# Kernel tuning notes

Hardware: AMD Instinct MI355X
Metric: run time of the kernel (lower is better)

## Reference

```python
import jax, jax.numpy as jnp
import numpy as np

N_NODES = 10000
N_EDGES = 160000
N_GRAPHS = 16
NUM_BASIS = 8
MIN_R = 0.25
MAX_R = 4.25
NUM_NEIGH = 10.0
SQRT3 = 3.0 ** 0.5


def setup_inputs() -> dict:
    key = jax.random.key(0)
    ks = jax.random.split(key, 24)
    f32 = jnp.float32
    g = lambda k, sh: jax.random.normal(k, sh, f32)
    inp = {}
    inp['x'] = g(ks[0], (N_NODES, 32))
    inp['node_attr'] = g(ks[1], (N_NODES, 16))
    inp['edge_src'] = jax.random.randint(ks[2], (N_EDGES,), 0, N_NODES)
    inp['edge_dst'] = jax.random.randint(ks[3], (N_EDGES,), 0, N_NODES)
    inp['edge_vec'] = g(ks[4], (N_EDGES, 3))
    inp['batch'] = jnp.sort(jax.random.randint(ks[5], (N_NODES,), 0, N_GRAPHS))
    # atom embedding Linear(32x0e -> 128x0e)
    inp['W_embed'] = g(ks[6], (32, 128))
    # conv1: in 128x0e, mid 128x0e+128x1o, out 128x0e+64x1o (gate input)
    inp['c1_lin1'] = g(ks[7], (128, 128))
    inp['c1_fc_w0'] = g(ks[8], (NUM_BASIS, 64))
    inp['c1_fc_w1'] = g(ks[9], (64, 64))
    inp['c1_fc_w2'] = g(ks[10], (64, 256))  # tp weight_numel = 128 + 128
    inp['c1_lin2_s'] = g(ks[11], (128, 128))
    inp['c1_lin2_v'] = g(ks[12], (128, 64))
    inp['c1_sc'] = g(ks[13], (128, 16, 128))  # FullyConnectedTP scalar path
    # conv2: in 64x0e+64x1o, mid 128x0e, out 128x0e
    inp['c2_lin1_s'] = g(ks[14], (64, 64))
    inp['c2_lin1_v'] = g(ks[15], (64, 64))
    inp['c2_fc_w0'] = g(ks[16], (NUM_BASIS, 64))
    inp['c2_fc_w1'] = g(ks[17], (64, 64))
    inp['c2_fc_w2'] = g(ks[18], (64, 128))  # tp weight_numel = 64 + 64
    inp['c2_lin2'] = g(ks[19], (128, 128))
    inp['c2_sc'] = g(ks[20], (64, 16, 128))
    # readout MLP 128 -> 128 -> 1
    inp['Wr1'] = g(ks[21], (128, 128))
    inp['Wr2'] = g(ks[22], (128, 1))
    return inp


def _lin(h, W):
    # e3nn Linear: normalized by 1/sqrt(fan_in)
    return h @ W * (W.shape[0] ** -0.5)


def _forward(x, node_attr, edge_src, edge_dst, edge_vec, batch,
             W_embed, c1_lin1, c1_fc_w0, c1_fc_w1, c1_fc_w2, c1_lin2_s,
             c1_lin2_v, c1_sc, c2_lin1_s, c2_lin1_v, c2_fc_w0, c2_fc_w1,
             c2_fc_w2, c2_lin2, c2_sc, Wr1, Wr2):
    silu = jax.nn.silu
    inv = NUM_NEIGH ** -0.5
    # ---- edge embeddings ----
    d = jnp.linalg.norm(edge_vec, axis=1)
    c = MAX_R - MIN_R
    xs = d - MIN_R
    safe = jnp.where(xs > 0, xs, 1.0)
    kpi = jnp.arange(1, NUM_BASIS + 1, dtype=jnp.float32) * jnp.pi
    bess = (2.0 / c) ** 0.5 * jnp.sin(kpi * safe[:, None] / c) / safe[:, None]
    mask = ((xs > 0) & (xs < c)).astype(jnp.float32)[:, None]
    edge_scalars = bess * mask * (NUM_BASIS ** 0.5)  # [E, 8]
    unit = edge_vec / jnp.where(d > 0, d, 1.0)[:, None]
    sh_v = SQRT3 * unit  # l=1 SH, component normalization (l=0 SH is 1)

    # ---- atom embedding ----
    s = _lin(x, W_embed)  # [N,128] 128x0e

    # ---- layer 1: Convolution(128x0e -> 128x0e+64x1o) + Gate ----
    h = _lin(s, c1_lin1)
    w = silu(_lin(edge_scalars, c1_fc_w0))
    w = silu(_lin(w, c1_fc_w1))
    w = _lin(w, c1_fc_w2)  # [E,256] per-edge TP weights
    w0, w1 = w[:, :128], w[:, 128:]
    hs = h[edge_src]  # gather [E,128]
    e_s = w0 * hs                                   # 0e x 0e -> 0e
    e_v = (w1 * hs)[:, :, None] * sh_v[:, None, :]  # 0e x 1o -> 1o  [E,128,3]
    n_s = jax.ops.segment_sum(e_s, edge_dst, num_segments=N_NODES) * inv
    n_v = jax.ops.segment_sum(e_v, edge_dst, num_segments=N_NODES) * inv
    out_s = _lin(n_s, c1_lin2_s)  # [N,128]: 64 scalars + 64 gates
    out_v = jnp.einsum('nui,uv->nvi', n_v, c1_lin2_v) * (128 ** -0.5)  # [N,64,3]
    sc1 = jnp.einsum('nu,nv,uvw->nw', s, node_attr, c1_sc) * ((128 * 16) ** -0.5)
    out_s = out_s + sc1
    g_s = silu(out_s[:, :64])                                  # gated scalars
    g_v = jax.nn.sigmoid(out_s[:, 64:])[:, :, None] * out_v    # gated 64x1o

    # ---- layer 2: final Convolution(64x0e+64x1o -> 128x0e) ----
    h_s = _lin(g_s, c2_lin1_s)
    h_v = jnp.einsum('nui,uv->nvi', g_v, c2_lin1_v) * (64 ** -0.5)
    w = silu(_lin(edge_scalars, c2_fc_w0))
    w = silu(_lin(w, c2_fc_w1))
    w = _lin(w, c2_fc_w2)  # [E,128]
    w0, w1 = w[:, :64], w[:, 64:]
    es = w0 * h_s[edge_src]                                           # 0e x 0e -> 0e
    ed = w1 * jnp.einsum('eui,ei->eu', h_v[edge_src], sh_v) * (3.0 ** -0.5)  # 1o x 1o -> 0e
    e_mid = jnp.concatenate([es, ed], axis=1)  # [E,128]
    n_mid = jax.ops.segment_sum(e_mid, edge_dst, num_segments=N_NODES) * inv
    out = _lin(n_mid, c2_lin2)
    sc2 = jnp.einsum('nu,nv,uvw->nw', g_s, node_attr, c2_sc) * ((64 * 16) ** -0.5)
    out = out + sc2  # [N,128]

    # ---- readout: mean pool per graph, MLP -> scalar per graph ----
    cnt = jax.ops.segment_sum(jnp.ones((N_NODES,), jnp.float32), batch,
                              num_segments=N_GRAPHS)
    pooled = jax.ops.segment_sum(out, batch, num_segments=N_GRAPHS)
    pooled = pooled / jnp.maximum(cnt, 1.0)[:, None]
    r = silu(_lin(pooled, Wr1))
    r = _lin(r, Wr2)  # [G,1]
    return r.reshape(-1)  # [G]


def reference(x, node_attr, edge_src, edge_dst, edge_vec, batch,
              W_embed, c1_lin1, c1_fc_w0, c1_fc_w1, c1_fc_w2, c1_lin2_s,
              c1_lin2_v, c1_sc, c2_lin1_s, c2_lin1_v, c2_fc_w0, c2_fc_w1,
              c2_fc_w2, c2_lin2, c2_sc, Wr1, Wr2):
    return _forward(x, node_attr, edge_src, edge_dst, edge_vec, batch,
                    W_embed, c1_lin1, c1_fc_w0, c1_fc_w1, c1_fc_w2, c1_lin2_s,
                    c1_lin2_v, c1_sc, c2_lin1_s, c2_lin1_v, c2_fc_w0, c2_fc_w1,
                    c2_fc_w2, c2_lin2, c2_sc, Wr1, Wr2)
```

## Files before the change

### kernel.cpp

```cpp
#include <hip/hip_runtime.h>
#include <hip/hip_fp16.h>

#define N_NODES 10000
#define N_EDGES 160000
#define N_GRAPHS 16

typedef __attribute__((ext_vector_type(8))) _Float16 f16x8;
typedef __attribute__((ext_vector_type(4))) float f32x4;
typedef __attribute__((ext_vector_type(4))) unsigned short u16x4;
typedef __attribute__((ext_vector_type(2))) unsigned short u16x2;
typedef unsigned int uint32;
typedef unsigned short u16;

#define OFF_ES8  0
#define OFF_SHV  (OFF_ES8 + N_EDGES*8)
#define OFF_S    (OFF_SHV + N_EDGES*3)
#define OFF_H    (OFF_S   + N_NODES*128)
#define OFF_GS   (OFF_H   + N_NODES*128)
#define OFF_HS   (OFF_GS  + N_NODES*64)
#define OFF_HV   (OFF_HS  + N_NODES*64)
#define OFF_NS   (OFF_HV  + N_NODES*192)
#define OFF_NV   (OFF_NS  + N_NODES*128)
#define OFF_NMID (OFF_NV  + N_NODES*384)
#define OFF_POOL (OFF_NMID+ N_NODES*128)
#define OFF_CNT  (OFF_POOL+ N_GRAPHS*128)
#define OFF_HIST (OFF_CNT + N_GRAPHS)
#define OFF_CURS (OFF_HIST+ N_NODES)
#define OFF_OFFS (OFF_CURS+ N_NODES)
#define OFF_FRAG (OFF_OFFS+ N_NODES + 16)
#define OFF_SLOT (OFF_FRAG+ 57344)
#define OFF_WBUF (OFF_SLOT+ N_EDGES)
#define WBUF_FLOATS ((size_t)N_EDGES*256)
#define WS_NEED_BYTES ((size_t)(OFF_WBUF + WBUF_FLOATS) * 4)

#define F_B1   0
#define F_B2   2048
#define F_B3   6144
#define F_B1b  22528
#define F_B2b  24576
#define F_B3b  28672
#define F_WE   36864
#define F_L1   40960
#define FRAG_TOT 57344

#define NF_WLS 0
#define NF_C1  16384
#define NF_W2  278528
#define NF_C2  294912
#define NF_LV  425984
#define NF_2S  434176
#define NF_2V  438272
#define NFRAG_TOT 442368

#define NM128 (N_NODES*128)

#define INV_SQRT32   0.17677669529663687f
#define INV_SQRT128  0.08838834764831845f
#define INV_SQRT8    0.3535533905932738f
#define INV_SQRT64   0.125f
#define INV_SQRT2048 0.022097086912079608f
#define INV_SQRT1024 0.03125f
#define INV_SQRT10   0.31622776601683794f
#define INV_SQRT3    0.5773502691896258f
#define SQRT3_C      1.7320508075688772f

__device__ __forceinline__ float siluf(float x){ return x / (1.f + __expf(-x)); }
__device__ __forceinline__ float sigf (float x){ return 1.f / (1.f + __expf(-x)); }
__device__ __forceinline__ u16 f2h(float x){ return __half_as_ushort(__float2half_rn(x)); }
__device__ __forceinline__ float h2f(u16 b){ return __half2float(__ushort_as_half(b)); }
__device__ __forceinline__ f16x8 cvt8(const float* __restrict__ p) {
  f32x4 v0 = *(const f32x4*)p;
  f32x4 v1 = *(const f32x4*)(p + 4);
  f16x8 r;
  r[0]=(_Float16)v0[0]; r[1]=(_Float16)v0[1]; r[2]=(_Float16)v0[2]; r[3]=(_Float16)v0[3];
  r[4]=(_Float16)v1[0]; r[5]=(_Float16)v1[1]; r[6]=(_Float16)v1[2]; r[7]=(_Float16)v1[3];
  return r;
}

__device__ __forceinline__ void geom_core(const float* __restrict__ ev,
                                          float* __restrict__ es, float* __restrict__ sv) {
  float vx = ev[0], vy = ev[1], vz = ev[2];
  float d  = sqrtf(vx*vx + vy*vy + vz*vz);
  float xs = d - 0.25f;
  bool  in = (xs > 0.f) && (xs < 4.0f);
  float safe = xs > 0.f ? xs : 1.f;
  float amp  = in ? 2.0f/safe : 0.f;
  const float PI4 = 0.7853981633974483f;
  #pragma unroll
  for (int k = 0; k < 8; ++k)
    es[k] = amp * sinf((float)(k+1) * PI4 * safe);
  float invd = d > 0.f ? 1.f/d : 1.f;
  sv[0] = SQRT3_C*vx*invd;
  sv[1] = SQRT3_C*vy*invd;
  sv[2] = SQRT3_C*vz*invd;
}

__global__ void k_geom_csr(const float* __restrict__ evec, const int* __restrict__ slot,
                           float* __restrict__ es8, float* __restrict__ shv) {
  int p = blockIdx.x*256 + threadIdx.x;
  if (p >= N_EDGES) return;
  int e = slot[p];
  float es[8], sv[3];
  geom_core(evec + (size_t)e*3, es, sv);
  #pragma unroll
  for (int k = 0; k < 8; ++k) es8[(size_t)p*8+k] = es[k];
  shv[(size_t)p*3+0] = sv[0]; shv[(size_t)p*3+1] = sv[1]; shv[(size_t)p*3+2] = sv[2];
}

__global__ void k_geom_id(const float* __restrict__ evec,
                          float* __restrict__ es8, float* __restrict__ shv) {
  int e = blockIdx.x*256 + threadIdx.x;
  if (e >= N_EDGES) return;
  float es[8], sv[3];
  geom_core(evec + (size_t)e*3, es, sv);
  #pragma unroll
  for (int k = 0; k < 8; ++k) es8[(size_t)e*8+k] = es[k];
  shv[(size_t)e*3+0] = sv[0]; shv[(size_t)e*3+1] = sv[1]; shv[(size_t)e*3+2] = sv[2];
}

__global__ void k_linear128(const float* __restrict__ A, const float* __restrict__ W,
                            float* __restrict__ O, int K, float scale, int total) {
  int t = blockIdx.x*256 + threadIdx.x;
  if (t >= total) return;
  int n = t >> 7, j = t & 127;
  const float* a = A + n*K;
  float a0=0.f,a1=0.f,a2=0.f,a3=0.f;
  for (int k = 0; k < K; k += 4) {
    a0 += a[k+0]*W[(k+0)*128+j];
    a1 += a[k+1]*W[(k+1)*128+j];
    a2 += a[k+2]*W[(k+2)*128+j];
    a3 += a[k+3]*W[(k+3)*128+j];
  }
  O[t] = (a0+a1+a2+a3)*scale;
}

__global__ void k_cnthist(const int* __restrict__ batch, const int* __restrict__ edst,
                          float* __restrict__ cnt, int* __restrict__ hist) {
  __shared__ int lc[N_GRAPHS];
  int t = threadIdx.x;
  if (t < N_GRAPHS) lc[t] = 0;
  __syncthreads();
  int i = blockIdx.x*256 + t;
  if (i < N_NODES) atomicAdd(&lc[batch[i]], 1);
  if (i < N_EDGES) atomicAdd(&hist[edst[i]], 1);
  __syncthreads();
  if (t < N_GRAPHS && lc[t] > 0) atomicAdd(&cnt[t], (float)lc[t]);
}

__global__ __launch_bounds__(1024) void k_scanp(const int* __restrict__ hist,
                                                int* __restrict__ offs) {
  __shared__ int wsum[16];
  const int t = threadIdx.x;
  const int lane = t & 63, w = t >> 6;
  const int base = t*10;
  int v[10]; int s = 0;
  #pragma unroll
  for (int i = 0; i < 10; ++i) {
    int idx = base + i;
    int x = (idx < N_NODES) ? hist[idx] : 0;
    s += x; v[i] = s;
  }
  int ws = s;
  #pragma unroll
  for (int d = 1; d < 64; d <<= 1) {
    int u = __shfl_up(ws, d);
    if (lane >= d) ws += u;
  }
  if (lane == 63) wsum[w] = ws;
  __syncthreads();
  if (w == 0) {
    int x = (lane < 16) ? wsum[lane] : 0;
    #pragma unroll
    for (int d = 1; d < 16; d <<= 1) {
      int u = __shfl_up(x, d);
      if (lane >= d) x += u;
    }
    if (lane < 16) wsum[lane] = x;
  }
  __syncthreads();
  int waveoff = (w > 0) ? wsum[w-1] : 0;
  int texcl = waveoff + ws - s;
  if (t == 0) offs[0] = 0;
  #pragma unroll
  for (int i = 0; i < 10; ++i) {
    int idx = base + i;
    if (idx < N_NODES) offs[idx+1] = texcl + v[i];
  }
}

__global__ void k_slot(const int* __restrict__ edst, const int* __restrict__ esrc,
                       const int* __restrict__ offs,
                       int* __restrict__ curs, int* __restrict__ slot,
                       int* __restrict__ esrcp) {
  int e = blockIdx.x*256 + threadIdx.x;
  if (e < N_EDGES) {
    int d = edst[e];
    int p = offs[d] + atomicAdd(&curs[d], 1);
    slot[p] = e;
    esrcp[p] = esrc[e];
  }
}

struct PD { const float* W; u16* dst; int Keff, N, KS, nElem; float scale; };
struct PD8 { PD d[8]; int nd; int tot; };

__global__ void k_prepmulti(PD8 ds) {
  int stride = gridDim.x*256;
  for (int t = blockIdx.x*256 + threadIdx.x; t < ds.tot; t += stride) {
    int rem = t, i = 0;
    while (i < ds.nd-1 && rem >= ds.d[i].nElem) { rem -= ds.d[i].nElem; ++i; }
    const PD p = ds.d[i];
    int j = rem & 7;
    int l = (rem >> 3) & 63;
    int rest = rem >> 9;
    int ks = rest % p.KS;
    int nf = rest / p.KS;
    int k   = ks*32 + (l >> 4)*8 + j;
    int col = nf*16 + (l & 15);
    float v = (k < p.Keff) ? p.W[(size_t)k*p.N + col]*p.scale : 0.f;
    p.dst[rem] = f2h(v);
  }
}

template<int NF3>
__global__ __launch_bounds__(256) void k_mlp(
    const float* __restrict__ es8,
    const u16* __restrict__ fb1, const u16* __restrict__ fb2,
    const u16* __restrict__ fb3, u16* __restrict__ wbuf) {
  __shared__ __align__(16) _Float16 route[4][2304];
  const int w = threadIdx.x >> 6, l = threadIdx.x & 63;
  const int lrow = l & 15, lhi = l >> 4;
  const int e0 = (blockIdx.x*4 + w)*32;
  _Float16* rt = route[w];
  constexpr int NQ = NF3/4;

  f16x8 a1[2];
  #pragma unroll
  for (int mt = 0; mt < 2; ++mt) {
    f16x8 z = {0,0,0,0,0,0,0,0};
    if (lhi == 0) z = cvt8(es8 + (size_t)(e0 + mt*16 + lrow)*8);
    a1[mt] = z;
  }

  f32x4 acc1[2][4];
  #pragma unroll
  for (int mt = 0; mt < 2; ++mt)
    #pragma unroll
    for (int nf = 0; nf < 4; ++nf) acc1[mt][nf] = (f32x4){0.f,0.f,0.f,0.f};
  #pragma unroll
  for (int nf = 0; nf < 4; ++nf) {
    f16x8 b = *(const f16x8*)(fb1 + nf*512 + l*8);
    #pragma unroll
    for (int mt = 0; mt < 2; ++mt)
      acc1[mt][nf] = __builtin_amdgcn_mfma_f32_16x16x32_f16(a1[mt], b, acc1[mt][nf], 0,0,0);
  }
  #pragma unroll
  for (int mt = 0; mt < 2; ++mt)
    #pragma unroll
    for (int nf = 0; nf < 4; ++nf)
      #pragma unroll
      for (int r = 0; r < 4; ++r) acc1[mt][nf][r] = siluf(acc1[mt][nf][r]);

  f16x8 a2[2][2];
  #pragma unroll
  for (int mt = 0; mt < 2; ++mt)
    #pragma unroll
    for (int nf = 0; nf < 4; ++nf)
      #pragma unroll
      for (int r = 0; r < 4; ++r)
        rt[(mt*16 + lhi*4 + r)*72 + nf*16 + lrow] = (_Float16)acc1[mt][nf][r];
  #pragma unroll
  for (int mt = 0; mt < 2; ++mt)
    #pragma unroll
    for (int ks = 0; ks < 2; ++ks)
      a2[mt][ks] = *(const f16x8*)&rt[(mt*16 + lrow)*72 + ks*32 + lhi*8];

  f32x4 acc2[2][4];
  #pragma unroll
  for (int mt = 0; mt < 2; ++mt)
    #pragma unroll
    for (int nf = 0; nf < 4; ++nf) acc2[mt][nf] = (f32x4){0.f,0.f,0.f,0.f};
  #pragma unroll
  for (int nf = 0; nf < 4; ++nf)
    #pragma unroll
    for (int ks = 0; ks < 2; ++ks) {
      f16x8 b = *(const f16x8*)(fb2 + (nf*2 + ks)*512 + l*8);
      #pragma unroll
      for (int mt = 0; mt < 2; ++mt)
        acc2[mt][nf] = __builtin_amdgcn_mfma_f32_16x16x32_f16(a2[mt][ks], b, acc2[mt][nf], 0,0,0);
    }
  #pragma unroll
  for (int mt = 0; mt < 2; ++mt)
    #pragma unroll
    for (int nf = 0; nf < 4; ++nf)
      #pragma unroll
      for (int r = 0; r < 4; ++r) acc2[mt][nf][r] = siluf(acc2[mt][nf][r]);

  f16x8 a3[2][2];
  #pragma unroll
  for (int mt = 0; mt < 2; ++mt)
    #pragma unroll
    for (int nf = 0; nf < 4; ++nf)
      #pragma unroll
      for (int r = 0; r < 4; ++r)
        rt[(mt*16 + lhi*4 + r)*72 + nf*16 + lrow] = (_Float16)acc2[mt][nf][r];
  #pragma unroll
  for (int mt = 0; mt < 2; ++mt)
    #pragma unroll
    for (int ks = 0; ks < 2; ++ks)
      a3[mt][ks] = *(const f16x8*)&rt[(mt*16 + lrow)*72 + ks*32 + lhi*8];

  #pragma unroll
  for (int cc = 0; cc < 4; ++cc) {
    f32x4 acc3[NQ][2];
    #pragma unroll
    for (int q = 0; q < NQ; ++q)
      #pragma unroll
      for (int mt = 0; mt < 2; ++mt) acc3[q][mt] = (f32x4){0.f,0.f,0.f,0.f};
    #pragma unroll
    for (int q = 0; q < NQ; ++q) {
      const int nf3 = q*4 + cc;
      #pragma unroll
      for (int ks = 0; ks < 2; ++ks) {
        f16x8 b = *(const f16x8*)(fb3 + ((size_t)nf3*2 + ks)*512 + l*8);
        #pragma unroll
        for (int mt = 0; mt < 2; ++mt)
          acc3[q][mt] = __builtin_amdgcn_mfma_f32_16x16x32_f16(a3[mt][ks], b, acc3[q][mt], 0,0,0);
      }
    }
    const int cbase = (cc*16 + lrow)*NQ;
    #pragma unroll
    for (int mt = 0; mt < 2; ++mt)
      #pragma unroll
      for (int r = 0; r < 4; ++r) {
        const size_t rowoff = (size_t)(e0 + mt*16 + lhi*4 + r)*(NF3*16) + cbase;
        if constexpr (NQ == 4) {
          u16x4 pk;
          #pragma unroll
          for (int q = 0; q < 4; ++q) pk[q] = f2h(acc3[q][mt][r]);
          *(u16x4*)(wbuf + rowoff) = pk;
        } else {
          u16x2 pk;
          #pragma unroll
          for (int q = 0; q < 2; ++q) pk[q] = f2h(acc3[q][mt][r]);
          *(u16x2*)(wbuf + rowoff) = pk;
        }
      }
  }
}

template<int KS, int NF>
__global__ __launch_bounds__(512, 4) void k_gemm(
    const float* __restrict__ A, int rstride, int M,
    const u16* __restrict__ fB, float* __restrict__ O) {
  __shared__ __align__(16) _Float16 lB[NF*KS*512];
  const int tid = threadIdx.x;
  const int w = tid >> 6, l = tid & 63;
  const int lrow = l & 15, lhi = l >> 4;
  const int n0 = blockIdx.x*128 + w*16;
  for (int i = tid; i < NF*KS*64; i += 512)
    *(f16x8*)&lB[(size_t)i*8] = *(const f16x8*)&fB[(size_t)i*8];
  f16x8 a[KS];
  {
    int row = n0 + lrow; if (row > M-1) row = M-1;
    #pragma unroll
    for (int ks = 0; ks < KS; ++ks)
      a[ks] = cvt8(A + (size_t)row*rstride + ks*32 + lhi*8);
  }
  __syncthreads();
  f32x4 acc[NF];
  #pragma unroll
  for (int nf = 0; nf < NF; ++nf) acc[nf] = (f32x4){0.f,0.f,0.f,0.f};
  #pragma unroll
  for (int nf = 0; nf < NF; ++nf)
    #pragma unroll
    for (int ks = 0; ks < KS; ++ks) {
      f16x8 b = *(const f16x8*)&lB[((size_t)(nf*KS + ks))*512 + l*8];
      acc[nf] = __builtin_amdgcn_mfma_f32_16x16x32_f16(a[ks], b, acc[nf], 0,0,0);
    }
  #pragma unroll
  for (int nf = 0; nf < NF; ++nf)
    #pragma unroll
    for (int r = 0; r < 4; ++r) {
      int row = n0 + lhi*4 + r;
      if (row < M) O[(size_t)row*(NF*16) + nf*16 + lrow] = acc[nf][r];
    }
}

template<int KSO>
__global__ __launch_bounds__(512, 4) void k_scp(
    const float* __restrict__ Ao, const float* __restrict__ na,
    const u16* __restrict__ fBc, float* __restrict__ part) {
  __shared__ __align__(16) _Float16 lB[KSO*4096];
  const int tid = threadIdx.x;
  const int w = tid >> 6, l = tid & 63;
  const int lrow = l & 15, lhi = l >> 4;
  const int n0 = blockIdx.x*128 + w*16;
  const int vp = blockIdx.y;

  f16x8 ao[KSO];
  {
    int row = n0 + lrow; if (row > N_NODES-1) row = N_NODES-1;
    #pragma unroll
    for (int ks = 0; ks < KSO; ++ks)
      ao[ks] = cvt8(Ao + (size_t)row*(KSO*32) + ks*32 + lhi*8);
  }

  f32x4 acc[8];
  #pragma unroll
  for (int nf = 0; nf < 8; ++nf) acc[nf] = (f32x4){0.f,0.f,0.f,0.f};

  #pragma unroll
  for (int c = 0; c < 2; ++c) {
    const int v = vp*2 + c;
    __syncthreads();
    for (int i = tid; i < KSO*512; i += 512) {
      int gl = i & 63;
      int rest = i >> 6;
      int ks = rest % KSO;
      int nf = rest / KSO;
      size_t src = (((size_t)(v*8 + nf)*KSO + ks)*64 + gl)*8;
      *(f16x8*)&lB[(size_t)i*8] = *(const f16x8*)&fBc[src];
    }
    __syncthreads();
    f32x4 dacc[8];
    #pragma unroll
    for (int nf = 0; nf < 8; ++nf) dacc[nf] = (f32x4){0.f,0.f,0.f,0.f};
    #pragma unroll
    for (int nf = 0; nf < 8; ++nf)
      #pragma unroll
      for (int ks = 0; ks < KSO; ++ks) {
        f16x8 b = *(const f16x8*)&lB[((size_t)(nf*KSO + ks))*512 + l*8];
        dacc[nf] = __builtin_amdgcn_mfma_f32_16x16x32_f16(ao[ks], b, dacc[nf], 0,0,0);
      }
    #pragma unroll
    for (int r = 0; r < 4; ++r) {
      int row = n0 + lhi*4 + r; if (row > N_NODES-1) row = N_NODES-1;
      float nav = na[(size_t)row*16 + v];
      #pragma unroll
      for (int nf = 0; nf < 8; ++nf) acc[nf][r] += nav * dacc[nf][r];
    }
  }

  float* pp = part + (size_t)vp*NM128;
  #pragma unroll
  for (int nf = 0; nf < 8; ++nf)
    #pragma unroll
    for (int r = 0; r < 4; ++r) {
      int row = n0 + lhi*4 + r;
      if (row < N_NODES) pp[(size_t)row*128 + nf*16 + lrow] = acc[nf][r];
    }
}

__global__ void k_redgate(const float* __restrict__ part, const float* __restrict__ ov,
                          float* __restrict__ gs_out, float* __restrict__ gv) {
  int t = blockIdx.x*256 + threadIdx.x;
  if (t >= N_NODES*64) return;
  int n = t >> 6, v = t & 63;
  float o1 = 0.f, o2 = 0.f;
  #pragma unroll
  for (int p = 0; p < 9; ++p) {
    const float* pp = part + (size_t)p*NM128 + (size_t)n*128;
    o1 += pp[v]; o2 += pp[64+v];
  }
  float g = siluf(o1), gate = sigf(o2);
  gs_out[(size_t)n*64+v] = g;
  gv[(size_t)n*192 + 0*64 + v] = gate*ov[(size_t)n*192 + 0*64 + v];
  gv[(size_t)n*192 + 1*64 + v] = gate*ov[(size_t)n*192 + 1*64 + v];
  gv[(size_t)n*192 + 2*64 + v] = gate*ov[(size_t)n*192 + 2*64 + v];
}

__global__ __launch_bounds__(128) void k_redpool(
    const float* __restrict__ part, const int* __restrict__ batch,
    float* __restrict__ pool) {
  const int j = threadIdx.x;
  const int n0 = blockIdx.x*4;
  float outv[4];
  #pragma unroll
  for (int nn = 0; nn < 4; ++nn) {
    float sv = 0.f;
    #pragma unroll
    for (int p = 0; p < 9; ++p)
      sv += part[(size_t)p*NM128 + (size_t)(n0+nn)*128 + j];
    outv[nn] = sv;
  }
  int b0 = batch[n0], b1 = batch[n0+1], b2 = batch[n0+2], b3 = batch[n0+3];
  float sum = outv[0]; int cur = b0;
  if (b1 == cur) sum += outv[1]; else { atomicAdd(&pool[cur*128+j], sum); cur = b1; sum = outv[1]; }
  if (b2 == cur) sum += outv[2]; else { atomicAdd(&pool[cur*128+j], sum); cur = b2; sum = outv[2]; }
  if (b3 == cur) sum += outv[3]; else { atomicAdd(&pool[cur*128+j], sum); cur = b3; sum = outv[3]; }
  atomicAdd(&pool[cur*128+j], sum);
}

__global__ __launch_bounds__(256) void k_gather1(
    const u16* __restrict__ wbuf, const float* __restrict__ shv,
    const int* __restrict__ esrcp, const int* __restrict__ offs,
    const float* __restrict__ h,
    float* __restrict__ n_s, float* __restrict__ n_v) {
  const int wave = threadIdx.x >> 6, lane = threadIdx.x & 63;
  const int n = blockIdx.x*4 + wave;
  if (n >= N_NODES) return;
  const int s0 = offs[n], s1 = offs[n+1];
  float ns0=0.f, ns1=0.f;
  float nv00=0.f,nv01=0.f,nv02=0.f, nv10=0.f,nv11=0.f,nv12=0.f;
  for (int s = s0; s < s1; ++s) {
    int src = esrcp[s];
    u16x4 wv = *(const u16x4*)(wbuf + (size_t)s*256 + lane*4);
    float c0 = h2f(wv[0]), c1 = h2f(wv[1]), c2 = h2f(wv[2]), c3 = h2f(wv[3]);
    float h0 = h[src*128+lane], h1 = h[src*128+64+lane];
    float sv0 = shv[(size_t)s*3+0], sv1 = shv[(size_t)s*3+1], sv2 = shv[(size_t)s*3+2];
    ns0 += c0*h0; ns1 += c1*h1;
    float t0 = c2*h0, t1 = c3*h1;
    nv00 += t0*sv0; nv01 += t0*sv1; nv02 += t0*sv2;
    nv10 += t1*sv0; nv11 += t1*sv1; nv12 += t1*sv2;
  }
  n_s[n*128+lane]    = ns0*INV_SQRT10;
  n_s[n*128+64+lane] = ns1*INV_SQRT10;
  float* nvp = n_v + (size_t)n*384;
  nvp[0*128+lane]    = nv00*INV_SQRT10;
  nvp[1*128+lane]    = nv01*INV_SQRT10;
  nvp[2*128+lane]    = nv02*INV_SQRT10;
  nvp[0*128+64+lane] = nv10*INV_SQRT10;
  nvp[1*128+64+lane] = nv11*INV_SQRT10;
  nvp[2*128+64+lane] = nv12*INV_SQRT10;
}

__global__ __launch_bounds__(256) void k_gather2(
    const u16* __restrict__ wbuf, const float* __restrict__ shv,
    const int* __restrict__ esrcp, const int* __restrict__ offs,
    const float* __restrict__ h_s, const float* __restrict__ h_v,
    float* __restrict__ n_mid) {
  const int wave = threadIdx.x >> 6, lane = threadIdx.x & 63;
  const int n = blockIdx.x*4 + wave;
  if (n >= N_NODES) return;
  const int s0 = offs[n], s1 = offs[n+1];
  float acc0 = 0.f, acc1 = 0.f;
  for (int s = s0; s < s1; ++s) {
    int src = esrcp[s];
    u16x2 wv = *(const u16x2*)(wbuf + (size_t)s*128 + lane*2);
    float w0 = h2f(wv[0]), w1 = h2f(wv[1]);
    float hs = h_s[src*64+lane];
    const float* hvp = h_v + (size_t)src*192;
    float sv0 = shv[(size_t)s*3+0], sv1 = shv[(size_t)s*3+1], sv2 = shv[(size_t)s*3+2];
    float dot = hvp[lane]*sv0 + hvp[64+lane]*sv1 + hvp[128+lane]*sv2;
    acc0 += w0*hs;
    acc1 += w1*dot;
  }
  n_mid[n*128+lane]    = acc0*INV_SQRT10;
  n_mid[n*128+64+lane] = acc1*INV_SQRT3*INV_SQRT10;
}

__global__ __launch_bounds__(512) void k_edge1_at(
    const float* __restrict__ es8, const float* __restrict__ shv,
    const int* __restrict__ esrc, const int* __restrict__ edst,
    const float* __restrict__ h,
    const float* __restrict__ W0, const float* __restrict__ W1, const float* __restrict__ W2,
    float* __restrict__ n_s, float* __restrict__ n_v) {
  __shared__ float lW0[512];
  __shared__ float lW1[4096];
  __shared__ float lW2[16384];
  __shared__ float lA[8][64];
  __shared__ float lB[8][64];
  for (int i = threadIdx.x; i < 512;   i += 512) lW0[i] = W0[i];
  for (int i = threadIdx.x; i < 4096;  i += 512) lW1[i] = W1[i];
  for (int i = threadIdx.x; i < 16384; i += 512) lW2[i] = W2[i];
  __syncthreads();
  const int wave = threadIdx.x >> 6, lane = threadIdx.x & 63;
  const int nw = gridDim.x * 8;
  const int e0 = blockIdx.x*8 + wave;
  const int iters = (N_EDGES + nw - 1) / nw;
  for (int it = 0; it < iters; ++it) {
    int e = e0 + it*nw;
    bool valid = e < N_EDGES;
    float a = 0.f, sv0=0.f, sv1=0.f, sv2=0.f;
    int src = 0, dst = 0;
    if (valid) {
      const float* ep = es8 + e*8;
      sv0 = shv[e*3+0]; sv1 = shv[e*3+1]; sv2 = shv[e*3+2];
      src = esrc[e]; dst = edst[e];
      a = ep[0]*lW0[lane]      + ep[1]*lW0[64+lane]  + ep[2]*lW0[128+lane] + ep[3]*lW0[192+lane]
        + ep[4]*lW0[256+lane]  + ep[5]*lW0[320+lane] + ep[6]*lW0[384+lane] + ep[7]*lW0[448+lane];
      a = siluf(a * INV_SQRT8);
    }
    lA[wave][lane] = a;
    __syncthreads();
    {
      float b0=0.f;
      #pragma unroll
      for (int k = 0; k < 64; ++k) b0 += lA[wave][k]*lW1[k*64+lane];
      lB[wave][lane] = siluf(b0 * INV_SQRT64);
    }
    __syncthreads();
    if (valid) {
      float c0=0.f,c1=0.f,c2=0.f,c3=0.f;
      #pragma unroll
      for (int k = 0; k < 64; ++k) {
        float bk = lB[wave][k];
        const float* r = lW2 + k*256;
        c0 += bk*r[lane]; c1 += bk*r[64+lane]; c2 += bk*r[128+lane]; c3 += bk*r[192+lane];
      }
      float hs0 = h[src*128 + lane];
      float hs1 = h[src*128 + 64 + lane];
      atomicAdd(&n_s[dst*128 + lane],      c0*INV_SQRT64*hs0*INV_SQRT10);
      atomicAdd(&n_s[dst*128 + 64 + lane], c1*INV_SQRT64*hs1*INV_SQRT10);
      float t0 = c2*INV_SQRT64*hs0*INV_SQRT10;
      float t1 = c3*INV_SQRT64*hs1*INV_SQRT10;
      float* nvp = n_v + dst*384;
      atomicAdd(nvp + lane*3+0, t0*sv0);
      atomicAdd(nvp + lane*3+1, t0*sv1);
      atomicAdd(nvp + lane*3+2, t0*sv2);
      atomicAdd(nvp + (64+lane)*3+0, t1*sv0);
      atomicAdd(nvp + (64+lane)*3+1, t1*sv1);
      atomicAdd(nvp + (64+lane)*3+2, t1*sv2);
    }
  }
}

__global__ __launch_bounds__(512) void k_edge2_at(
    const float* __restrict__ es8, const float* __restrict__ shv,
    const int* __restrict__ esrc, const int* __restrict__ edst,
    const float* __restrict__ h_s, const float* __restrict__ h_v,
    const float* __restrict__ W0, const float* __restrict__ W1, const float* __restrict__ W2,
    float* __restrict__ n_mid) {
  __shared__ float lW0[512];
  __shared__ float lW1[4096];
  __shared__ float lW2[8192];
  __shared__ float lA[8][64];
// ... 169 lines not shown
    acc[0] += l_nm[k]*w; acc[1] += l_nm[128+k]*w;
    acc[2] += l_nm[256+k]*w; acc[3] += l_nm[384+k]*w;
  }
  float acc2[4] = {0.f,0.f,0.f,0.f};
  for (int vt = 0; vt < 16; vt += 4) {
    float a0[4],a1[4],a2[4],a3[4];
    #pragma unroll
    for (int n = 0; n < 4; ++n) {
      a0[n]=l_na[n*16+vt]; a1[n]=l_na[n*16+vt+1];
      a2[n]=l_na[n*16+vt+2]; a3[n]=l_na[n*16+vt+3];
    }
    for (int u = 0; u < 64; ++u) {
      const float* cp = Csc + (u*16+vt)*128 + j;
      float c0=cp[0], c1=cp[128], c2=cp[256], c3=cp[384];
      float s0=l_gs[u], s1=l_gs[64+u], s2=l_gs[128+u], s3=l_gs[192+u];
      acc2[0] += s0*(a0[0]*c0 + a1[0]*c1 + a2[0]*c2 + a3[0]*c3);
      acc2[1] += s1*(a0[1]*c0 + a1[1]*c1 + a2[1]*c2 + a3[1]*c3);
      acc2[2] += s2*(a0[2]*c0 + a1[2]*c1 + a2[2]*c2 + a3[2]*c3);
      acc2[3] += s3*(a0[3]*c0 + a1[3]*c1 + a2[3]*c2 + a3[3]*c3);
    }
  }
  float outv[4];
  #pragma unroll
  for (int n = 0; n < 4; ++n)
    outv[n] = acc[n]*INV_SQRT128 + acc2[n]*INV_SQRT1024;
  int b0 = batch[n0], b1 = batch[n0+1], b2 = batch[n0+2], b3 = batch[n0+3];
  float sum = outv[0]; int cur = b0;
  if (b1 == cur) sum += outv[1]; else { atomicAdd(&pool[cur*128+j], sum); cur = b1; sum = outv[1]; }
  if (b2 == cur) sum += outv[2]; else { atomicAdd(&pool[cur*128+j], sum); cur = b2; sum = outv[2]; }
  if (b3 == cur) sum += outv[3]; else { atomicAdd(&pool[cur*128+j], sum); cur = b3; sum = outv[3]; }
  atomicAdd(&pool[cur*128+j], sum);
}

__global__ __launch_bounds__(128) void k_head(
    const float* __restrict__ pool, const float* __restrict__ cnt,
    const float* __restrict__ Wr1, const float* __restrict__ Wr2,
    float* __restrict__ out) {
  __shared__ float lp[128];
  __shared__ float wsum[2];
  const int j = threadIdx.x;
  const int g = blockIdx.x;
  float inv = 1.f / fmaxf(cnt[g], 1.f);
  lp[j] = pool[(size_t)g*128 + j]*inv;
  __syncthreads();
  float acc = 0.f;
  for (int k = 0; k < 128; ++k) acc += lp[k]*Wr1[k*128+j];
  float val = siluf(acc*INV_SQRT128) * Wr2[j];
  #pragma unroll
  for (int d = 32; d > 0; d >>= 1) val += __shfl_down(val, d);
  if ((j & 63) == 0) wsum[j >> 6] = val;
  __syncthreads();
  if (j == 0) out[g] = (wsum[0] + wsum[1]) * INV_SQRT128;
}

extern "C" void kernel_launch(void* const* d_in, const int* in_sizes, int n_in,
                              void* d_out, int out_size, void* d_ws, size_t ws_size,
                              hipStream_t stream) {
  const float* x         = (const float*)d_in[0];
  const float* node_attr = (const float*)d_in[1];
  const int*   esrc      = (const int*)d_in[2];
  const int*   edst      = (const int*)d_in[3];
  const float* evec      = (const float*)d_in[4];
  const int*   batch     = (const int*)d_in[5];
  const float* W_embed   = (const float*)d_in[6];
  const float* c1_lin1   = (const float*)d_in[7];
  const float* c1_fc_w0  = (const float*)d_in[8];
  const float* c1_fc_w1  = (const float*)d_in[9];
  const float* c1_fc_w2  = (const float*)d_in[10];
  const float* c1_lin2_s = (const float*)d_in[11];
  const float* c1_lin2_v = (const float*)d_in[12];
  const float* c1_sc     = (const float*)d_in[13];
  const float* c2_lin1_s = (const float*)d_in[14];
  const float* c2_lin1_v = (const float*)d_in[15];
  const float* c2_fc_w0  = (const float*)d_in[16];
  const float* c2_fc_w1  = (const float*)d_in[17];
  const float* c2_fc_w2  = (const float*)d_in[18];
  const float* c2_lin2   = (const float*)d_in[19];
  const float* c2_sc     = (const float*)d_in[20];
  const float* Wr1       = (const float*)d_in[21];
  const float* Wr2       = (const float*)d_in[22];

  float* ws    = (float*)d_ws;
  float* es8   = ws + OFF_ES8;
  float* shv   = ws + OFF_SHV;
  float* s_    = ws + OFF_S;
  float* h_    = ws + OFF_H;
  float* gs_   = ws + OFF_GS;
  float* hs_   = ws + OFF_HS;
  float* hv_   = ws + OFF_HV;
  float* ns_   = ws + OFF_NS;
  float* nv_   = ws + OFF_NV;
  float* nmid_ = ws + OFF_NMID;
  float* pool_ = ws + OFF_POOL;
  float* cnt_  = ws + OFF_CNT;
  int*   hist_ = (int*)(ws + OFF_HIST);
  int*   curs_ = (int*)(ws + OFF_CURS);
  int*   offs_ = (int*)(ws + OFF_OFFS);
  u16*   frag_ = (u16*)(ws + OFF_FRAG);
  int*   slot_ = (int*)(ws + OFF_SLOT);
  float* wbuf_ = ws + OFF_WBUF;
  u16*   wb16_ = (u16*)wbuf_;

  float* out1_  = wbuf_ + (size_t)N_EDGES*128;
  u16*   nfrag_ = (u16*)(out1_ + (size_t)NM128);
  float* part_  = out1_ + (size_t)NM128 + NFRAG_TOT/2;
  float* ov_    = part_ + (size_t)9*NM128;
  int*   esrcp_ = (int*)(ov_ + (size_t)N_NODES*192);
  float* gv_    = nv_;

  const bool big = ws_size >= WS_NEED_BYTES;

  if (big) {
    hipMemsetAsync(pool_, 0, (size_t)(OFF_OFFS - OFF_POOL)*sizeof(float), stream);
    k_cnthist<<<(N_EDGES+255)/256, 256, 0, stream>>>(batch, edst, cnt_, hist_);
    k_scanp<<<1, 1024, 0, stream>>>(hist_, offs_);
    k_slot<<<(N_EDGES+255)/256, 256, 0, stream>>>(edst, esrc, offs_, curs_, slot_, esrcp_);
    k_geom_csr<<<(N_EDGES+255)/256, 256, 0, stream>>>(evec, slot_, es8, shv);

    {
      PD8 m{};
      m.d[0] = {c1_fc_w0, frag_ + F_B1,  8,  64,  1, 2048,  INV_SQRT8};
      m.d[1] = {c1_fc_w1, frag_ + F_B2,  64, 64,  2, 4096,  INV_SQRT64};
      m.d[2] = {c1_fc_w2, frag_ + F_B3,  64, 256, 2, 16384, INV_SQRT64};
      m.d[3] = {c2_fc_w0, frag_ + F_B1b, 8,  64,  1, 2048,  INV_SQRT8};
      m.d[4] = {c2_fc_w1, frag_ + F_B2b, 64, 64,  2, 4096,  INV_SQRT64};
      m.d[5] = {c2_fc_w2, frag_ + F_B3b, 64, 128, 2, 8192,  INV_SQRT64};
      m.d[6] = {W_embed,  frag_ + F_WE,  32, 128, 1, 4096,  INV_SQRT32};
      m.d[7] = {c1_lin1,  frag_ + F_L1,  128,128, 4, 16384, INV_SQRT128};
      m.nd = 8; m.tot = FRAG_TOT;
      k_prepmulti<<<224, 256, 0, stream>>>(m);
    }

    k_gemm<1,8><<<79, 512, 0, stream>>>(x,  32,  N_NODES, frag_ + F_WE, s_);
    k_gemm<4,8><<<79, 512, 0, stream>>>(s_, 128, N_NODES, frag_ + F_L1, h_);

    k_mlp<16><<<1250, 256, 0, stream>>>(es8, frag_ + F_B1, frag_ + F_B2, frag_ + F_B3, wb16_);
    k_gather1<<<(N_NODES+3)/4, 256, 0, stream>>>(wb16_, shv, esrcp_, offs_, h_, ns_, nv_);

    {
      PD8 m{};
      m.d[0] = {c1_lin2_s, nfrag_ + NF_WLS, 128, 128,  4, 16384,  INV_SQRT128};
      m.d[1] = {c1_sc,     nfrag_ + NF_C1,  128, 2048, 4, 262144, INV_SQRT2048};
      m.d[2] = {c2_lin2,   nfrag_ + NF_W2,  128, 128,  4, 16384,  INV_SQRT128};
      m.d[3] = {c2_sc,     nfrag_ + NF_C2,  64,  2048, 2, 131072, INV_SQRT1024};
      m.d[4] = {c1_lin2_v, nfrag_ + NF_LV,  128, 64,   4, 8192,   INV_SQRT128};
      m.d[5] = {c2_lin1_s, nfrag_ + NF_2S,  64,  64,   2, 4096,   INV_SQRT64};
      m.d[6] = {c2_lin1_v, nfrag_ + NF_2V,  64,  64,   2, 4096,   INV_SQRT64};
      m.nd = 7; m.tot = NFRAG_TOT;
      k_prepmulti<<<864, 256, 0, stream>>>(m);
    }

    k_gemm<4,8><<<79, 512, 0, stream>>>(ns_, 128, N_NODES, nfrag_ + NF_WLS, part_ + (size_t)8*NM128);
    k_scp<4><<<dim3(79,8), 512, 0, stream>>>(s_, node_attr, nfrag_ + NF_C1, part_);
    k_gemm<4,4><<<235, 512, 0, stream>>>(nv_, 128, N_NODES*3, nfrag_ + NF_LV, ov_);
    k_redgate<<<(N_NODES*64+255)/256, 256, 0, stream>>>(part_, ov_, gs_, gv_);
    k_gemm<2,4><<<79, 512, 0, stream>>>(gs_, 64, N_NODES, nfrag_ + NF_2S, hs_);
    k_gemm<2,4><<<235, 512, 0, stream>>>(gv_, 64, N_NODES*3, nfrag_ + NF_2V, hv_);

    k_mlp<8><<<1250, 256, 0, stream>>>(es8, frag_ + F_B1b, frag_ + F_B2b, frag_ + F_B3b, wb16_);
    k_gather2<<<(N_NODES+3)/4, 256, 0, stream>>>(wb16_, shv, esrcp_, offs_, hs_, hv_, nmid_);

    k_gemm<4,8><<<79, 512, 0, stream>>>(nmid_, 128, N_NODES, nfrag_ + NF_W2, part_ + (size_t)8*NM128);
    k_scp<2><<<dim3(79,8), 512, 0, stream>>>(gs_, node_attr, nfrag_ + NF_C2, part_);
    k_redpool<<<N_NODES/4, 128, 0, stream>>>(part_, batch, pool_);
  } else {
    hipMemsetAsync(ns_, 0, (size_t)(OFF_HIST - OFF_NS)*sizeof(float), stream);
    k_geom_id<<<N_EDGES/256, 256, 0, stream>>>(evec, es8, shv);
    k_linear128<<<(N_NODES*128)/256, 256, 0, stream>>>(x,  W_embed, s_, 32,  INV_SQRT32,  N_NODES*128);
    k_linear128<<<(N_NODES*128)/256, 256, 0, stream>>>(s_, c1_lin1, h_, 128, INV_SQRT128, N_NODES*128);
    k_cnthist<<<(N_EDGES+255)/256, 256, 0, stream>>>(batch, edst, cnt_, hist_);
    k_edge1_at<<<256, 512, 0, stream>>>(es8, shv, esrc, edst, h_,
                                        c1_fc_w0, c1_fc_w1, c1_fc_w2, ns_, nv_);
    k_node1<<<N_NODES/4, 128, 0, stream>>>(ns_, nv_, s_, node_attr,
                                           c1_lin2_s, c1_lin2_v, c1_sc,
                                           c2_lin1_s, c2_lin1_v, gs_, hs_, hv_);
    k_edge2_at<<<512, 512, 0, stream>>>(es8, shv, esrc, edst, hs_, hv_,
                                        c2_fc_w0, c2_fc_w1, c2_fc_w2, nmid_);
    k_node2<<<N_NODES/4, 128, 0, stream>>>(nmid_, gs_, node_attr, batch,
                                           c2_lin2, c2_sc, pool_);
  }

  k_head<<<N_GRAPHS, 128, 0, stream>>>(pool_, cnt_, Wr1, Wr2, (float*)d_out);
}
```

Baseline: 275.4 us.

## Fuse slot and geometry kernels, merge weight prep, store gathered features as fp16

Merges the CSR slot assignment with edge geometry so each edge is handled in one kernel, and writes the radial basis as fp16 so the MLP kernel loads it directly. Combines the two weight-fragment preparation launches into one. GEMMs that produce node features read by the edge gathers (h, hs, hv) now write fp16, halving the bytes the random-access gathers fetch. This trades precision in the gathered features for less memory traffic and fewer launches.

Measured after the change: 261.3 us (median of 2 runs). 5.1% less time.

```diff
diff --git a/kernel.cpp b/kernel.cpp
--- a/kernel.cpp
+++ b/kernel.cpp
@@ -95,15 +95,22 @@
   sv[2] = SQRT3_C*vz*invd;
 }
 
-__global__ void k_geom_csr(const float* __restrict__ evec, const int* __restrict__ slot,
-                           float* __restrict__ es8, float* __restrict__ shv) {
-  int p = blockIdx.x*256 + threadIdx.x;
-  if (p >= N_EDGES) return;
-  int e = slot[p];
+__global__ void k_slotgeom(const int* __restrict__ edst, const int* __restrict__ esrc,
+                           const float* __restrict__ evec, const int* __restrict__ offs,
+                           int* __restrict__ curs, int* __restrict__ esrcp,
+                           u16* __restrict__ es8h, float* __restrict__ shv) {
+  int e = blockIdx.x*256 + threadIdx.x;
+  if (e >= N_EDGES) return;
+  int d = edst[e];
+  int p = offs[d] + atomicAdd(&curs[d], 1);
+  esrcp[p] = esrc[e];
   float es[8], sv[3];
   geom_core(evec + (size_t)e*3, es, sv);
-  #pragma unroll
-  for (int k = 0; k < 8; ++k) es8[(size_t)p*8+k] = es[k];
+  u16x4 a, b;
+  #pragma unroll
+  for (int k = 0; k < 4; ++k) { a[k] = f2h(es[k]); b[k] = f2h(es[k+4]); }
+  *(u16x4*)(es8h + (size_t)p*8)     = a;
+  *(u16x4*)(es8h + (size_t)p*8 + 4) = b;
   shv[(size_t)p*3+0] = sv[0]; shv[(size_t)p*3+1] = sv[1]; shv[(size_t)p*3+2] = sv[2];
 }
 
@@ -188,23 +195,10 @@
   }
 }
 
-__global__ void k_slot(const int* __restrict__ edst, const int* __restrict__ esrc,
-                       const int* __restrict__ offs,
-                       int* __restrict__ curs, int* __restrict__ slot,
-                       int* __restrict__ esrcp) {
-  int e = blockIdx.x*256 + threadIdx.x;
-  if (e < N_EDGES) {
-    int d = edst[e];
-    int p = offs[d] + atomicAdd(&curs[d], 1);
-    slot[p] = e;
-    esrcp[p] = esrc[e];
-  }
-}
-
 struct PD { const float* W; u16* dst; int Keff, N, KS, nElem; float scale; };
-struct PD8 { PD d[8]; int nd; int tot; };
-
-__global__ void k_prepmulti(PD8 ds) {
+struct PDS { PD d[15]; int nd; int tot; };
+
+__global__ void k_prepmulti(PDS ds) {
   int stride = gridDim.x*256;
   for (int t = blockIdx.x*256 + threadIdx.x; t < ds.tot; t += stride) {
     int rem = t, i = 0;
@@ -224,7 +218,7 @@
 
 template<int NF3>
 __global__ __launch_bounds__(256) void k_mlp(
-    const float* __restrict__ es8,
+    const u16* __restrict__ es8h,
     const u16* __restrict__ fb1, const u16* __restrict__ fb2,
     const u16* __restrict__ fb3, u16* __restrict__ wbuf) {
   __shared__ __align__(16) _Float16 route[4][2304];
@@ -238,7 +232,7 @@
   #pragma unroll
   for (int mt = 0; mt < 2; ++mt) {
     f16x8 z = {0,0,0,0,0,0,0,0};
-    if (lhi == 0) z = cvt8(es8 + (size_t)(e0 + mt*16 + lrow)*8);
+    if (lhi == 0) z = *(const f16x8*)(es8h + (size_t)(e0 + mt*16 + lrow)*8);
     a1[mt] = z;
   }
 
@@ -349,10 +343,10 @@
   }
 }
 
-template<int KS, int NF>
+template<int KS, int NF, bool F16OUT>
 __global__ __launch_bounds__(512, 4) void k_gemm(
     const float* __restrict__ A, int rstride, int M,
-    const u16* __restrict__ fB, float* __restrict__ O) {
+    const u16* __restrict__ fB, void* __restrict__ Ov) {
   __shared__ __align__(16) _Float16 lB[NF*KS*512];
   const int tid = threadIdx.x;
   const int w = tid >> 6, l = tid & 63;
@@ -383,7 +377,11 @@
     #pragma unroll
     for (int r = 0; r < 4; ++r) {
       int row = n0 + lhi*4 + r;
-      if (row < M) O[(size_t)row*(NF*16) + nf*16 + lrow] = acc[nf][r];
+      if (row < M) {
+        size_t idx = (size_t)row*(NF*16) + nf*16 + lrow;
+        if constexpr (F16OUT) ((u16*)Ov)[idx] = f2h(acc[nf][r]);
+        else                  ((float*)Ov)[idx] = acc[nf][r];
+      }
     }
 }
 
@@ -495,7 +493,7 @@
 __global__ __launch_bounds__(256) void k_gather1(
     const u16* __restrict__ wbuf, const float* __restrict__ shv,
     const int* __restrict__ esrcp, const int* __restrict__ offs,
-    const float* __restrict__ h,
+    const u16* __restrict__ h16,
     float* __restrict__ n_s, float* __restrict__ n_v) {
   const int wave = threadIdx.x >> 6, lane = threadIdx.x & 63;
   const int n = blockIdx.x*4 + wave;
@@ -507,7 +505,7 @@
     int src = esrcp[s];
     u16x4 wv = *(const u16x4*)(wbuf + (size_t)s*256 + lane*4);
     float c0 = h2f(wv[0]), c1 = h2f(wv[1]), c2 = h2f(wv[2]), c3 = h2f(wv[3]);
-    float h0 = h[src*128+lane], h1 = h[src*128+64+lane];
+    float h0 = h2f(h16[(size_t)src*128+lane]), h1 = h2f(h16[(size_t)src*128+64+lane]);
     float sv0 = shv[(size_t)s*3+0], sv1 = shv[(size_t)s*3+1], sv2 = shv[(size_t)s*3+2];
     ns0 += c0*h0; ns1 += c1*h1;
     float t0 = c2*h0, t1 = c3*h1;
@@ -528,7 +526,7 @@
 __global__ __launch_bounds__(256) void k_gather2(
     const u16* __restrict__ wbuf, const float* __restrict__ shv,
     const int* __restrict__ esrcp, const int* __restrict__ offs,
-    const float* __restrict__ h_s, const float* __restrict__ h_v,
+    const u16* __restrict__ hs16, const u16* __restrict__ hv16,
     float* __restrict__ n_mid) {
   const int wave = threadIdx.x >> 6, lane = threadIdx.x & 63;
   const int n = blockIdx.x*4 + wave;
@@ -539,10 +537,10 @@
     int src = esrcp[s];
     u16x2 wv = *(const u16x2*)(wbuf + (size_t)s*128 + lane*2);
     float w0 = h2f(wv[0]), w1 = h2f(wv[1]);
-    float hs = h_s[src*64+lane];
-    const float* hvp = h_v + (size_t)src*192;
+    float hs = h2f(hs16[(size_t)src*64+lane]);
+    const u16* hvp = hv16 + (size_t)src*192;
     float sv0 = shv[(size_t)s*3+0], sv1 = shv[(size_t)s*3+1], sv2 = shv[(size_t)s*3+2];
-    float dot = hvp[lane]*sv0 + hvp[64+lane]*sv1 + hvp[128+lane]*sv2;
+    float dot = h2f(hvp[lane])*sv0 + h2f(hvp[64+lane])*sv1 + h2f(hvp[128+lane])*sv2;
     acc0 += w0*hs;
     acc1 += w1*dot;
   }
@@ -878,12 +876,16 @@
 
   float* ws    = (float*)d_ws;
   float* es8   = ws + OFF_ES8;
+  u16*   es8h_ = (u16*)es8;
   float* shv   = ws + OFF_SHV;
   float* s_    = ws + OFF_S;
   float* h_    = ws + OFF_H;
+  u16*   h16_  = (u16*)h_;
   float* gs_   = ws + OFF_GS;
   float* hs_   = ws + OFF_HS;
+  u16*   hs16_ = (u16*)hs_;
   float* hv_   = ws + OFF_HV;
+  u16*   hv16_ = (u16*)hv_;
   float* ns_   = ws + OFF_NS;
   float* nv_   = ws + OFF_NV;
   float* nmid_ = ws + OFF_NMID;
@@ -893,7 +895,7 @@
   int*   curs_ = (int*)(ws + OFF_CURS);
   int*   offs_ = (int*)(ws + OFF_OFFS);
   u16*   frag_ = (u16*)(ws + OFF_FRAG);
-  int*   slot_ = (int*)(ws + OFF_SLOT);
+  int*   esrcp_= (int*)(ws + OFF_SLOT);
   float* wbuf_ = ws + OFF_WBUF;
   u16*   wb16_ = (u16*)wbuf_;
 
@@ -901,7 +903,6 @@
   u16*   nfrag_ = (u16*)(out1_ + (size_t)NM128);
   float* part_  = out1_ + (size_t)NM128 + NFRAG_TOT/2;
   float* ov_    = part_ + (size_t)9*NM128;
-  int*   esrcp_ = (int*)(ov_ + (size_t)N_NODES*192);
   float* gv_    = nv_;
 
   const bool big = ws_size >= WS_NEED_BYTES;
@@ -910,53 +911,47 @@
     hipMemsetAsync(pool_, 0, (size_t)(OFF_OFFS - OFF_POOL)*sizeof(float), stream);
     k_cnthist<<<(N_EDGES+255)/256, 256, 0, stream>>>(batch, edst, cnt_, hist_);
     k_scanp<<<1, 1024, 0, stream>>>(hist_, offs_);
-    k_slot<<<(N_EDGES+255)/256, 256, 0, stream>>>(edst, esrc, offs_, curs_, slot_, esrcp_);
-    k_geom_csr<<<(N_EDGES+255)/256, 256, 0, stream>>>(evec, slot_, es8, shv);
+    k_slotgeom<<<(N_EDGES+255)/256, 256, 0, stream>>>(edst, esrc, evec, offs_,
+                                                      curs_, esrcp_, es8h_, shv);
 
     {
-      PD8 m{};
-      m.d[0] = {c1_fc_w0, frag_ + F_B1,  8,  64,  1, 2048,  INV_SQRT8};
-      m.d[1] = {c1_fc_w1, frag_ + F_B2,  64, 64,  2, 4096,  INV_SQRT64};
-      m.d[2] = {c1_fc_w2, frag_ + F_B3,  64, 256, 2, 16384, INV_SQRT64};
-      m.d[3] = {c2_fc_w0, frag_ + F_B1b, 8,  64,  1, 2048,  INV_SQRT8};
-      m.d[4] = {c2_fc_w1, frag_ + F_B2b, 64, 64,  2, 4096,  INV_SQRT64};
-      m.d[5] = {c2_fc_w2, frag_ + F_B3b, 64, 128, 2, 8192,  INV_SQRT64};
-      m.d[6] = {W_embed,  frag_ + F_WE,  32, 128, 1, 4096,  INV_SQRT32};
-      m.d[7] = {c1_lin1,  frag_ + F_L1,  128,128, 4, 16384, INV_SQRT128};
-      m.nd = 8; m.tot = FRAG_TOT;
-      k_prepmulti<<<224, 256, 0, stream>>>(m);
-    }
-
-    k_gemm<1,8><<<79, 512, 0, stream>>>(x,  32,  N_NODES, frag_ + F_WE, s_);
-    k_gemm<4,8><<<79, 512, 0, stream>>>(s_, 128, N_NODES, frag_ + F_L1, h_);
-
-    k_mlp<16><<<1250, 256, 0, stream>>>(es8, frag_ + F_B1, frag_ + F_B2, frag_ + F_B3, wb16_);
-    k_gather1<<<(N_NODES+3)/4, 256, 0, stream>>>(wb16_, shv, esrcp_, offs_, h_, ns_, nv_);
-
-    {
-      PD8 m{};
-      m.d[0] = {c1_lin2_s, nfrag_ + NF_WLS, 128, 128,  4, 16384,  INV_SQRT128};
-      m.d[1] = {c1_sc,     nfrag_ + NF_C1,  128, 2048, 4, 262144, INV_SQRT2048};
-      m.d[2] = {c2_lin2,   nfrag_ + NF_W2,  128, 128,  4, 16384,  INV_SQRT128};
-      m.d[3] = {c2_sc,     nfrag_ + NF_C2,  64,  2048, 2, 131072, INV_SQRT1024};
-      m.d[4] = {c1_lin2_v, nfrag_ + NF_LV,  128, 64,   4, 8192,   INV_SQRT128};
-      m.d[5] = {c2_lin1_s, nfrag_ + NF_2S,  64,  64,   2, 4096,   INV_SQRT64};
-      m.d[6] = {c2_lin1_v, nfrag_ + NF_2V,  64,  64,   2, 4096,   INV_SQRT64};
-      m.nd = 7; m.tot = NFRAG_TOT;
-      k_prepmulti<<<864, 256, 0, stream>>>(m);
-    }
-
-    k_gemm<4,8><<<79, 512, 0, stream>>>(ns_, 128, N_NODES, nfrag_ + NF_WLS, part_ + (size_t)8*NM128);
+      PDS m{};
+      m.d[0]  = {c1_fc_w0,  frag_  + F_B1,   8,   64,   1, 2048,   INV_SQRT8};
+      m.d[1]  = {c1_fc_w1,  frag_  + F_B2,   64,  64,   2, 4096,   INV_SQRT64};
+      m.d[2]  = {c1_fc_w2,  frag_  + F_B3,   64,  256,  2, 16384,  INV_SQRT64};
+      m.d[3]  = {c2_fc_w0,  frag_  + F_B1b,  8,   64,   1, 2048,   INV_SQRT8};
+      m.d[4]  = {c2_fc_w1,  frag_  + F_B2b,  64,  64,   2, 4096,   INV_SQRT64};
+      m.d[5]  = {c2_fc_w2,  frag_  + F_B3b,  64,  128,  2, 8192,   INV_SQRT64};
+      m.d[6]  = {W_embed,   frag_  + F_WE,   32,  128,  1, 4096,   INV_SQRT32};
+      m.d[7]  = {c1_lin1,   frag_  + F_L1,   128, 128,  4, 16384,  INV_SQRT128};
+      m.d[8]  = {c1_lin2_s, nfrag_ + NF_WLS, 128, 128,  4, 16384,  INV_SQRT128};
+      m.d[9]  = {c1_sc,     nfrag_ + NF_C1,  128, 2048, 4, 262144, INV_SQRT2048};
+      m.d[10] = {c2_lin2,   nfrag_ + NF_W2,  128, 128,  4, 16384,  INV_SQRT128};
+      m.d[11] = {c2_sc,     nfrag_ + NF_C2,  64,  2048, 2, 131072, INV_SQRT1024};
+      m.d[12] = {c1_lin2_v, nfrag_ + NF_LV,  128, 64,   4, 8192,   INV_SQRT128};
+      m.d[13] = {c2_lin1_s, nfrag_ + NF_2S,  64,  64,   2, 4096,   INV_SQRT64};
+      m.d[14] = {c2_lin1_v, nfrag_ + NF_2V,  64,  64,   2, 4096,   INV_SQRT64};
+      m.nd = 15; m.tot = FRAG_TOT + NFRAG_TOT;
+      k_prepmulti<<<976, 256, 0, stream>>>(m);
+    }
+
+    k_gemm<1,8,false><<<79, 512, 0, stream>>>(x,  32,  N_NODES, frag_ + F_WE, s_);
+    k_gemm<4,8,true ><<<79, 512, 0, stream>>>(s_, 128, N_NODES, frag_ + F_L1, h16_);
+
+    k_mlp<16><<<1250, 256, 0, stream>>>(es8h_, frag_ + F_B1, frag_ + F_B2, frag_ + F_B3, wb16_);
+    k_gather1<<<(N_NODES+3)/4, 256, 0, stream>>>(wb16_, shv, esrcp_, offs_, h16_, ns_, nv_);
+
+    k_gemm<4,8,false><<<79, 512, 0, stream>>>(ns_, 128, N_NODES, nfrag_ + NF_WLS, part_ + (size_t)8*NM128);
     k_scp<4><<<dim3(79,8), 512, 0, stream>>>(s_, node_attr, nfrag_ + NF_C1, part_);
-    k_gemm<4,4><<<235, 512, 0, stream>>>(nv_, 128, N_NODES*3, nfrag_ + NF_LV, ov_);
+    k_gemm<4,4,false><<<235, 512, 0, stream>>>(nv_, 128, N_NODES*3, nfrag_ + NF_LV, ov_);
     k_redgate<<<(N_NODES*64+255)/256, 256, 0, stream>>>(part_, ov_, gs_, gv_);
-    k_gemm<2,4><<<79, 512, 0, stream>>>(gs_, 64, N_NODES, nfrag_ + NF_2S, hs_);
-    k_gemm<2,4><<<235, 512, 0, stream>>>(gv_, 64, N_NODES*3, nfrag_ + NF_2V, hv_);
-
-    k_mlp<8><<<1250, 256, 0, stream>>>(es8, frag_ + F_B1b, frag_ + F_B2b, frag_ + F_B3b, wb16_);
-    k_gather2<<<(N_NODES+3)/4, 256, 0, stream>>>(wb16_, shv, esrcp_, offs_, hs_, hv_, nmid_);
-
-    k_gemm<4,8><<<79, 512, 0, stream>>>(nmid_, 128, N_NODES, nfrag_ + NF_W2, part_ + (size_t)8*NM128);
+    k_gemm<2,4,true><<<79, 512, 0, stream>>>(gs_, 64, N_NODES, nfrag_ + NF_2S, hs16_);
+    k_gemm<2,4,true><<<235, 512, 0, stream>>>(gv_, 64, N_NODES*3, nfrag_ + NF_2V, hv16_);
+
+    k_mlp<8><<<1250, 256, 0, stream>>>(es8h_, frag_ + F_B1b, frag_ + F_B2b, frag_ + F_B3b, wb16_);
+    k_gather2<<<(N_NODES+3)/4, 256, 0, stream>>>(wb16_, shv, esrcp_, offs_, hs16_, hv16_, nmid_);
+
+    k_gemm<4,8,false><<<79, 512, 0, stream>>>(nmid_, 128, N_NODES, nfrag_ + NF_W2, part_ + (size_t)8*NM128);
     k_scp<2><<<dim3(79,8), 512, 0, stream>>>(gs_, node_attr, nfrag_ + NF_C2, part_);
     k_redpool<<<N_NODES/4, 128, 0, stream>>>(part_, batch, pool_);
   } else {
```
